# Performance work log

Hardware: AMD Instinct MI355X
Metric: run time of the kernel (lower is better)

The kernel has to match this reference:

```python
import jax, jax.numpy as jnp
import numpy as np

EPS = 1e-5  # torch InstanceNorm2d default eps

def _instance_norm(x):
    # Normalize each (b, c) plane over spatial dims, biased variance (torch semantics).
    mean = jnp.mean(x, axis=(-2, -1), keepdims=True)
    var = jnp.mean(jnp.square(x - mean), axis=(-2, -1), keepdims=True)
    return (x - mean) * jax.lax.rsqrt(var + EPS)

def setup_inputs() -> dict:
    key = jax.random.key(0)
    k1, k2 = jax.random.split(key)
    B, C, H, W = 64, 1, 512, 512
    x1 = jax.random.normal(k1, (B, C, H, W), dtype=jnp.float32)
    x2 = jax.random.normal(k2, (B, C, H, W), dtype=jnp.float32)
    return {"x1": x1, "x2": x2}

def reference(x1, x2):
    b, c, h, w = x2.shape
    x1n = _instance_norm(x1)
    x2n = _instance_norm(x2)
    # per-pair dot product over C*H*W, shape [B, 1, 1]
    scores = jnp.einsum('bchw,bchw->b', x1n, x2n).reshape(b, 1, 1)
    scores = scores / (h * w * c)
    return scores
```

## Files before the change

kernel.cpp:

```cpp
#include <hip/hip_runtime.h>
#include <math.h>


#define HW        262144
#define PLANE_F4  65536
#define BPB       32
#define THREADS   256
#define CHUNK     (PLANE_F4 / BPB)
#define NBATCH    64
#define EPSN      1e-5

#define ACC(a, c)                                                     \
    s1  += (a.x + a.y) + (a.z + a.w);                                 \
    s2  += (c.x + c.y) + (c.z + c.w);                                 \
    s11 = fmaf(a.x, a.x, s11); s11 = fmaf(a.y, a.y, s11);             \
    s11 = fmaf(a.z, a.z, s11); s11 = fmaf(a.w, a.w, s11);             \
    s22 = fmaf(c.x, c.x, s22); s22 = fmaf(c.y, c.y, s22);             \
    s22 = fmaf(c.z, c.z, s22); s22 = fmaf(c.w, c.w, s22);             \
    s12 = fmaf(a.x, c.x, s12); s12 = fmaf(a.y, c.y, s12);             \
    s12 = fmaf(a.z, c.z, s12); s12 = fmaf(a.w, c.w, s12);

__global__ __launch_bounds__(THREADS, 8) void xcorr_partial(
        const float4* __restrict__ x1, const float4* __restrict__ x2,
        double* __restrict__ part) {
    const int b  = blockIdx.x >> 5;
    const int jb = blockIdx.x & (BPB - 1);
    const int base = jb * CHUNK + threadIdx.x;
    const float4* q1 = x1 + (long long)b * PLANE_F4 + base;
    const float4* q2 = x2 + (long long)b * PLANE_F4 + base;

    float s1 = 0.f, s2 = 0.f, s11 = 0.f, s22 = 0.f, s12 = 0.f;

    {
        const float4 a0 = q1[0 * THREADS];
        const float4 a1 = q1[1 * THREADS];
        const float4 a2 = q1[2 * THREADS];
        const float4 a3 = q1[3 * THREADS];
        const float4 c0 = q2[0 * THREADS];
        const float4 c1 = q2[1 * THREADS];
        const float4 c2 = q2[2 * THREADS];
        const float4 c3 = q2[3 * THREADS];
        ACC(a0, c0) ACC(a1, c1) ACC(a2, c2) ACC(a3, c3)
    }
    {
        const float4 a0 = q1[4 * THREADS];
        const float4 a1 = q1[5 * THREADS];
        const float4 a2 = q1[6 * THREADS];
        const float4 a3 = q1[7 * THREADS];
        const float4 c0 = q2[4 * THREADS];
        const float4 c1 = q2[5 * THREADS];
        const float4 c2 = q2[6 * THREADS];
        const float4 c3 = q2[7 * THREADS];
        ACC(a0, c0) ACC(a1, c1) ACC(a2, c2) ACC(a3, c3)
    }

    double d0 = s1, d1 = s2, d2 = s11, d3 = s22, d4 = s12;
    #pragma unroll
    for (int off = 32; off > 0; off >>= 1) {
        d0 += __shfl_down(d0, off, 64);
        d1 += __shfl_down(d1, off, 64);
        d2 += __shfl_down(d2, off, 64);
        d3 += __shfl_down(d3, off, 64);
        d4 += __shfl_down(d4, off, 64);
    }
    __shared__ double lds[4][5];
    const int lane = threadIdx.x & 63;
    const int wv   = threadIdx.x >> 6;
    if (lane == 0) {
        lds[wv][0] = d0; lds[wv][1] = d1; lds[wv][2] = d2;
        lds[wv][3] = d3; lds[wv][4] = d4;
    }
    __syncthreads();
    if (threadIdx.x == 0) {
        double* o = part + (long long)blockIdx.x * 5;
        #pragma unroll
        for (int i = 0; i < 5; ++i)
            o[i] = (lds[0][i] + lds[1][i]) + (lds[2][i] + lds[3][i]);
    }
}

__global__ __launch_bounds__(256) void xcorr_final(
        const double* __restrict__ part, float* __restrict__ out) {
    const int tid = threadIdx.x;
    const int b = tid >> 2;
    const int g = tid & 3;
    const double* p = part + (long long)b * BPB * 5 + (long long)g * 8 * 5;
    double s0 = 0, s1 = 0, s2 = 0, s3 = 0, s4 = 0;
    #pragma unroll
    for (int j = 0; j < 8; ++j) {
        s0 += p[j * 5 + 0];
        s1 += p[j * 5 + 1];
        s2 += p[j * 5 + 2];
        s3 += p[j * 5 + 3];
        s4 += p[j * 5 + 4];
    }
    #pragma unroll
    for (int off = 2; off > 0; off >>= 1) {
        s0 += __shfl_down(s0, off, 64);
        s1 += __shfl_down(s1, off, 64);
        s2 += __shfl_down(s2, off, 64);
        s3 += __shfl_down(s3, off, 64);
        s4 += __shfl_down(s4, off, 64);
    }
    if (g == 0) {
        const double N  = (double)HW;
        const double m1 = s0 / N, m2 = s1 / N;
        const double v1 = s2 / N - m1 * m1;
        const double v2 = s3 / N - m2 * m2;
        const double cv = s4 / N - m1 * m2;
        out[b] = (float)(cv / sqrt((v1 + EPSN) * (v2 + EPSN)));
    }
}

extern "C" void kernel_launch(void* const* d_in, const int* in_sizes, int n_in,
                              void* d_out, int out_size, void* d_ws, size_t ws_size,
                              hipStream_t stream) {
    const float4* x1 = (const float4*)d_in[0];
    const float4* x2 = (const float4*)d_in[1];
    double* part = (double*)d_ws;
    float* out = (float*)d_out;

    xcorr_partial<<<NBATCH * BPB, THREADS, 0, stream>>>(x1, x2, part);
    xcorr_final<<<1, 256, 0, stream>>>(part, out);
}
```

Measured before the change: 28.54 us.

## Fuse final reduction into partial kernel via fixed-point atomics and last-block finish

Removes the separate final-reduction kernel. Each block adds its five partial sums, quantized to 64-bit fixed point, into per-batch atomic accumulators, and the last block per batch (found with an atomic counter) computes the output. A memset is added to zero the accumulators and counters each call. This trades one kernel launch for a memset plus atomics, and fixed-point quantization may lose precision.

```diff
diff --git a/kernel.cpp b/kernel.cpp
--- a/kernel.cpp
+++ b/kernel.cpp
@@ -9,6 +9,8 @@
 #define CHUNK     (PLANE_F4 / BPB)
 #define NBATCH    64
 #define EPSN      1e-5
+#define QSCALE    4294967296.0
+#define QINV      (1.0 / 4294967296.0)
 
 #define ACC(a, c)                                                     \
     s1  += (a.x + a.y) + (a.z + a.w);                                 \
@@ -20,9 +22,11 @@
     s12 = fmaf(a.x, c.x, s12); s12 = fmaf(a.y, c.y, s12);             \
     s12 = fmaf(a.z, c.z, s12); s12 = fmaf(a.w, c.w, s12);
 
-__global__ __launch_bounds__(THREADS, 8) void xcorr_partial(
+__global__ __launch_bounds__(THREADS, 8) void xcorr_fused(
         const float4* __restrict__ x1, const float4* __restrict__ x2,
-        double* __restrict__ part) {
+        unsigned long long* __restrict__ acc,
+        unsigned int* __restrict__ cnt,
+        float* __restrict__ out) {
     const int b  = blockIdx.x >> 5;
     const int jb = blockIdx.x & (BPB - 1);
     const int base = jb * CHUNK + threadIdx.x;
@@ -71,44 +75,35 @@
         lds[wv][3] = d3; lds[wv][4] = d4;
     }
     __syncthreads();
+
     if (threadIdx.x == 0) {
-        double* o = part + (long long)blockIdx.x * 5;
-        #pragma unroll
-        for (int i = 0; i < 5; ++i)
-            o[i] = (lds[0][i] + lds[1][i]) + (lds[2][i] + lds[3][i]);
-    }
-}
+        const double r0 = (lds[0][0] + lds[1][0]) + (lds[2][0] + lds[3][0]);
+        const double r1 = (lds[0][1] + lds[1][1]) + (lds[2][1] + lds[3][1]);
+        const double r2 = (lds[0][2] + lds[1][2]) + (lds[2][2] + lds[3][2]);
+        const double r3 = (lds[0][3] + lds[1][3]) + (lds[2][3] + lds[3][3]);
+        const double r4 = (lds[0][4] + lds[1][4]) + (lds[2][4] + lds[3][4]);
 
-__global__ __launch_bounds__(256) void xcorr_final(
-        const double* __restrict__ part, float* __restrict__ out) {
-    const int tid = threadIdx.x;
-    const int b = tid >> 2;
-    const int g = tid & 3;
-    const double* p = part + (long long)b * BPB * 5 + (long long)g * 8 * 5;
-    double s0 = 0, s1 = 0, s2 = 0, s3 = 0, s4 = 0;
-    #pragma unroll
-    for (int j = 0; j < 8; ++j) {
-        s0 += p[j * 5 + 0];
-        s1 += p[j * 5 + 1];
-        s2 += p[j * 5 + 2];
-        s3 += p[j * 5 + 3];
-        s4 += p[j * 5 + 4];
-    }
-    #pragma unroll
-    for (int off = 2; off > 0; off >>= 1) {
-        s0 += __shfl_down(s0, off, 64);
-        s1 += __shfl_down(s1, off, 64);
-        s2 += __shfl_down(s2, off, 64);
-        s3 += __shfl_down(s3, off, 64);
-        s4 += __shfl_down(s4, off, 64);
-    }
-    if (g == 0) {
-        const double N  = (double)HW;
-        const double m1 = s0 / N, m2 = s1 / N;
-        const double v1 = s2 / N - m1 * m1;
-        const double v2 = s3 / N - m2 * m2;
-        const double cv = s4 / N - m1 * m2;
-        out[b] = (float)(cv / sqrt((v1 + EPSN) * (v2 + EPSN)));
+        unsigned long long* a = acc + (long long)b * 5;
+        atomicAdd(&a[0], (unsigned long long)(long long)llrint(r0 * QSCALE));
+        atomicAdd(&a[1], (unsigned long long)(long long)llrint(r1 * QSCALE));
+        atomicAdd(&a[2], (unsigned long long)(long long)llrint(r2 * QSCALE));
+        atomicAdd(&a[3], (unsigned long long)(long long)llrint(r3 * QSCALE));
+        atomicAdd(&a[4], (unsigned long long)(long long)llrint(r4 * QSCALE));
+        asm volatile("s_waitcnt vmcnt(0)" ::: "memory");
+        const unsigned int old = atomicAdd(&cnt[b], 1u);
+        if (old == BPB - 1) {
+            const double t0 = (double)(long long)atomicAdd(&a[0], 0ULL) * QINV;
+            const double t1 = (double)(long long)atomicAdd(&a[1], 0ULL) * QINV;
+            const double t2 = (double)(long long)atomicAdd(&a[2], 0ULL) * QINV;
+            const double t3 = (double)(long long)atomicAdd(&a[3], 0ULL) * QINV;
+            const double t4 = (double)(long long)atomicAdd(&a[4], 0ULL) * QINV;
+            const double N  = (double)HW;
+            const double m1 = t0 / N, m2 = t1 / N;
+            const double v1 = t2 / N - m1 * m1;
+            const double v2 = t3 / N - m2 * m2;
+            const double cv = t4 / N - m1 * m2;
+            out[b] = (float)(cv / sqrt((v1 + EPSN) * (v2 + EPSN)));
+        }
     }
 }
 
@@ -117,9 +112,11 @@
                               hipStream_t stream) {
     const float4* x1 = (const float4*)d_in[0];
     const float4* x2 = (const float4*)d_in[1];
-    double* part = (double*)d_ws;
+    unsigned long long* acc = (unsigned long long*)d_ws;
+    unsigned int* cnt = (unsigned int*)((char*)d_ws + NBATCH * 5 * sizeof(unsigned long long));
     float* out = (float*)d_out;
 
-    xcorr_partial<<<NBATCH * BPB, THREADS, 0, stream>>>(x1, x2, part);
-    xcorr_final<<<1, 256, 0, stream>>>(part, out);
+    hipMemsetAsync(d_ws, 0, NBATCH * 5 * sizeof(unsigned long long)
+                            + NBATCH * sizeof(unsigned int), stream);
+    xcorr_fused<<<NBATCH * BPB, THREADS, 0, stream>>>(x1, x2, acc, cnt, out);
 }
```

New measurement: 37.10 us. 30.0% more time.
